# Kernel optimization log

Measured on AMD Instinct MI355X. Metric: run time of the kernel, lower is better.

The kernel has to match this reference:

```python
import jax, jax.numpy as jnp
import numpy as np

K = 3          # conv kernel size
STRIDE = 1     # conv stride (SAME padding)
ITERS = 3      # DR routing iterations
EPS = 1e-9     # squash epsilon


def squash(s, axis):
    # v = ||s||^2 / (1 + ||s||^2) * s / ||s||   (DR squash)
    sq = jnp.sum(s * s, axis=axis, keepdims=True)
    return (sq / (1.0 + sq)) * s * jax.lax.rsqrt(sq + EPS)


def setup_inputs() -> dict:
    key = jax.random.key(0)
    k1, k2, k3 = jax.random.split(key, 3)
    b, h, w, iCaps, iPose = 8, 12, 12, 32, 16
    oCaps, oPose = 32, 16
    x = jax.random.normal(k1, (b, h, w, iCaps, iPose), dtype=jnp.float32)
    # Wa: [kk*iCaps, oCaps, iPose, oPose] (leading 1 of the TF weight is dropped)
    fan = K * K * iCaps * iPose
    W = jax.random.normal(k2, (K * K * iCaps, oCaps, iPose, oPose), dtype=jnp.float32) * np.float32(np.sqrt(2.0 / fan))
    # biases: [oCaps, oPose] (TF shape [1,1,oCaps,oPose,1], broadcastable)
    biases = jax.random.normal(k3, (oCaps, oPose), dtype=jnp.float32) * 0.05
    return {"x": x, "W": W, "biases": biases}


def _kernel_tile(x2d):
    # im2col for SAME padding, stride 1.  x2d: (b, h, w, C) -> (b, h, w, k*k, C)
    b, h, w, C = x2d.shape
    pad = K // 2
    xp = jnp.pad(x2d, ((0, 0), (pad, pad), (pad, pad), (0, 0)))
    patches = jnp.stack(
        [xp[:, i:i + h, j:j + w, :] for i in range(K) for j in range(K)], axis=3
    )
    return patches  # (b, h, w, k*k, C)


def reference(x, W, biases):
    b, h, w, iCaps, iPose = x.shape
    iC = K * K * iCaps
    oC, oP = biases.shape

    # 1. kernel_tile: gather k*k neighborhoods
    patches = _kernel_tile(x.reshape(b, h, w, iCaps * iPose))      # (b,h,w,kk,iCaps*iPose)
    u = patches.reshape(b * h * w, iC, iPose)                       # (bx, iC, iPose)

    # 2. transform_view (vector capsules): votes[n,i,c,:] = u[n,i,:] @ W[i,c,:,:]
    votes = jnp.einsum('nip,icpq->nicq', u, W)                      # (bx, iC, oC, oP)

    # 3. DR routing
    bx = votes.shape[0]
    logits = jnp.zeros((bx, iC, oC), dtype=votes.dtype)
    v = None
    for ii in range(ITERS):
        c = jax.nn.softmax(logits, axis=2)                          # coupling coeffs over oCaps
        s = jnp.einsum('nic,nicq->ncq', c, votes) + biases          # (bx, oC, oP)
        v = squash(s, axis=2)
        if ii < ITERS - 1:
            logits = logits + jnp.einsum('nicq,ncq->nic', votes, v)  # agreement

    return v.reshape(b, h, w, oC, oP)
```

## Files before the change

kernel.cpp:

```cpp
#include <hip/hip_runtime.h>
#include <stdint.h>

typedef unsigned short ushort_t;

#define KK3 3
#define IC 32
#define IP 16
#define OC 32
#define OP 16
#define NI 288
#define HH 12
#define WWW 12
#define NTOT 1152
#define CQ 512
#define EPSQ 1e-9f
#define RWAVES 4
#define RSTEPS 36
#define NIP 144

typedef __attribute__((ext_vector_type(8))) short bf16x8;
typedef __attribute__((ext_vector_type(4))) float f32x4;

__device__ __forceinline__ float bf_lo(unsigned u) { return __uint_as_float(u << 16); }
__device__ __forceinline__ float bf_hi(unsigned u) { return __uint_as_float(u & 0xffff0000u); }
__device__ __forceinline__ ushort_t f2bf(float f) {
    unsigned u = __float_as_uint(f);
    return (ushort_t)((u + 0x7fffu + ((u >> 16) & 1u)) >> 16);
}

__global__ __launch_bounds__(64) void pack_kernel(
    const float* __restrict__ W, ushort_t* __restrict__ Wp)
{
    const int blk = blockIdx.x;
    const int ip = blk >> 5;
    const int c = blk & 31;
    const int l = threadIdx.x;
    const int i = ip * 2 + ((l >> 5) & 1);
    const int p0 = ((l >> 4) & 1) * 8;
    const int q = l & 15;
    const float* src = W + (((size_t)(i * 32 + c) * 16 + p0) * 16 + q);
    union { ushort_t s[8]; uint4 u4; } o;
#pragma unroll
    for (int j = 0; j < 8; ++j) o.s[j] = f2bf(src[(size_t)j * 16]);
    *(uint4*)(Wp + ((size_t)blk * 64 + l) * 8) = o.u4;
}

__global__ __launch_bounds__(256) void s0_gemm_kernel(
    const float* __restrict__ x, const ushort_t* __restrict__ Wp,
    float* __restrict__ s0_pre)
{
    __shared__ float red[4][512];

    const int t = threadIdx.x;
    const int wv = t >> 6;
    const int l = t & 63;
    const int pxt = blockIdx.x;
    const int ctb = blockIdx.y * 2;
    const int px = pxt * 16 + (l & 15);
    const int b = px / (HH * WWW);
    const int rem = px % (HH * WWW);
    const int y = rem / WWW;
    const int xx = rem % WWW;
    const int ioff = (l >> 5) & 1;
    const int p0 = ((l >> 4) & 1) * 8;

    f32x4 acc0 = (f32x4){0.f, 0.f, 0.f, 0.f};
    f32x4 acc1 = (f32x4){0.f, 0.f, 0.f, 0.f};

    const int ip0 = wv * (NIP / 4);
    for (int k = 0; k < NIP / 4; ++k) {
        const int ip = ip0 + k;
        const int i = ip * 2 + ioff;
        const int ky = i / (KK3 * IC);
        const int kx = (i / IC) % KK3;
        const int ic = i & (IC - 1);
        const int sy = y + ky - 1;
        const int sx = xx + kx - 1;
        union { ushort_t s[8]; bf16x8 v; } ua;
        if (sy >= 0 && sy < HH && sx >= 0 && sx < WWW) {
            const float* s = x + ((((size_t)b * HH + sy) * WWW + sx) * IC + ic) * IP + p0;
            const float4 v0 = *(const float4*)s;
            const float4 v1 = *(const float4*)(s + 4);
            ua.s[0] = f2bf(v0.x); ua.s[1] = f2bf(v0.y); ua.s[2] = f2bf(v0.z); ua.s[3] = f2bf(v0.w);
            ua.s[4] = f2bf(v1.x); ua.s[5] = f2bf(v1.y); ua.s[6] = f2bf(v1.z); ua.s[7] = f2bf(v1.w);
        } else {
#pragma unroll
            for (int j = 0; j < 8; ++j) ua.s[j] = 0;
        }
        const bf16x8 b0 = *(const bf16x8*)(Wp + (((size_t)ip * 32 + ctb) * 64 + l) * 8);
        const bf16x8 b1 = *(const bf16x8*)(Wp + (((size_t)ip * 32 + ctb + 1) * 64 + l) * 8);
        acc0 = __builtin_amdgcn_mfma_f32_16x16x32_bf16(ua.v, b0, acc0, 0, 0, 0);
        acc1 = __builtin_amdgcn_mfma_f32_16x16x32_bf16(ua.v, b1, acc1, 0, 0, 0);
    }

    {
        const int row = (l >> 4) * 4;
        const int col = l & 15;
#pragma unroll
        for (int r = 0; r < 4; ++r) {
            red[wv][(row + r) * 16 + col] = acc0[r];
            red[wv][256 + (row + r) * 16 + col] = acc1[r];
        }
    }
    __syncthreads();
#pragma unroll
    for (int rep = 0; rep < 2; ++rep) {
        const int k = t + rep * 256;
        const float v = (red[0][k] + red[1][k]) + (red[2][k] + red[3][k]);
        const int ct = k >> 8;
        const int row = (k >> 4) & 15;
        const int col = k & 15;
        s0_pre[(size_t)(pxt * 16 + row) * CQ + (size_t)(ctb + ct) * 16 + col] = v;
    }
}

__global__ __launch_bounds__(128) void votes_kernel(
    const float* __restrict__ x, const float* __restrict__ Wg,
    ushort_t* __restrict__ votes, int nStart, int nCount)
{
    __shared__ float u_lds[64][IP];

    const int i = blockIdx.x;
    const int tileBase = blockIdx.y * 64;
    const int nC = min(64, nCount - tileBase);
    const int t = threadIdx.x;
    const int c = t >> 2;
    const int qq = t & 3;

    const int ky = i / (KK3 * IC);
    const int kx = (i / IC) % KK3;
    const int ic = i % IC;

    {
        const int nl = t >> 1;
        const int ph = (t & 1) * 8;
        if (nl < nC) {
            const int n = nStart + tileBase + nl;
            const int b = n / (HH * WWW);
            const int rem = n % (HH * WWW);
            const int y = rem / WWW;
            const int xx = rem % WWW;
            const int sy = y + ky - 1;
            const int sx = xx + kx - 1;
            float4 v0 = make_float4(0.f, 0.f, 0.f, 0.f), v1 = v0;
            if (sy >= 0 && sy < HH && sx >= 0 && sx < WWW) {
                const float* src = x + ((((size_t)b * HH + sy) * WWW + sx) * IC + ic) * IP + ph;
                v0 = *(const float4*)(src);
                v1 = *(const float4*)(src + 4);
            }
            *(float4*)&u_lds[nl][ph] = v0;
            *(float4*)&u_lds[nl][ph + 4] = v1;
        }
    }

    float4 w[IP];
    {
        const float* wb = Wg + ((size_t)i * OC + c) * (IP * OP) + qq * 4;
#pragma unroll
        for (int p = 0; p < IP; ++p) w[p] = *(const float4*)(wb + p * OP);
    }
    __syncthreads();

    ushort_t* vb = votes + ((size_t)tileBase * NI + i) * CQ + c * OP + qq * 4;
    for (int nl = 0; nl < nC; ++nl) {
        const float4 u0 = *(const float4*)&u_lds[nl][0];
        const float4 u1 = *(const float4*)&u_lds[nl][4];
        const float4 u2 = *(const float4*)&u_lds[nl][8];
        const float4 u3 = *(const float4*)&u_lds[nl][12];
        float a0 = 0.f, a1 = 0.f, a2 = 0.f, a3 = 0.f;
#define ACC(uf, pp)                                         \
        a0 = fmaf(uf, w[pp].x, a0); a1 = fmaf(uf, w[pp].y, a1); \
        a2 = fmaf(uf, w[pp].z, a2); a3 = fmaf(uf, w[pp].w, a3);
        ACC(u0.x, 0)  ACC(u0.y, 1)  ACC(u0.z, 2)  ACC(u0.w, 3)
        ACC(u1.x, 4)  ACC(u1.y, 5)  ACC(u1.z, 6)  ACC(u1.w, 7)
        ACC(u2.x, 8)  ACC(u2.y, 9)  ACC(u2.z, 10) ACC(u2.w, 11)
        ACC(u3.x, 12) ACC(u3.y, 13) ACC(u3.z, 14) ACC(u3.w, 15)
#undef ACC
        ushort4 st;
        st.x = f2bf(a0); st.y = f2bf(a1); st.z = f2bf(a2); st.w = f2bf(a3);
        *(ushort4*)vb = st;
        vb += (size_t)NI * CQ;
    }
}

#define UNPACK16(A, B)                                                     \
    const float f0 = bf_lo(A.x), f1 = bf_hi(A.x), f2 = bf_lo(A.y),         \
                f3 = bf_hi(A.y), f4 = bf_lo(A.z), f5 = bf_hi(A.z),         \
                f6 = bf_lo(A.w), f7 = bf_hi(A.w), f8 = bf_lo(B.x),         \
                f9 = bf_hi(B.x), f10 = bf_lo(B.y), f11 = bf_hi(B.y),       \
                f12 = bf_lo(B.z), f13 = bf_hi(B.z), f14 = bf_lo(B.w),      \
                f15 = bf_hi(B.w);

__global__ __launch_bounds__(256) void route_kernel(
    const ushort_t* __restrict__ votes, const float* __restrict__ s0_pre,
    const float* __restrict__ bias, float* __restrict__ out, int nStart)
{
    __shared__ float lg_lds[NI * OC];
    __shared__ float sPart[RWAVES][CQ];
    __shared__ float s_sh[CQ];
    __shared__ float v_sh[CQ];
    __shared__ float fac_sh[OC];

    const int bn = blockIdx.x;
    const int t = threadIdx.x;
    const int wv = t >> 6;
    const int l = t & 63;
    const int isub = l >> 5;
    const int c = l & 31;
    const int iBase = 2 * wv + isub;

    const ushort_t* pbase = votes + (size_t)bn * NI * CQ + (size_t)iBase * CQ + c * OP;
    const size_t stepB = (size_t)8 * CQ;

#pragma unroll
    for (int rep = 0; rep < 2; ++rep) {
        const int k = t + rep * 256;
        s_sh[k] = fmaf(s0_pre[(size_t)(nStart + bn) * CQ + k], 1.0f / OC, bias[k]);
    }
    __syncthreads();
    if (t < OC) {
        float sq = 0.f;
#pragma unroll
        for (int q = 0; q < OP; ++q) { const float s = s_sh[t * OP + q]; sq = fmaf(s, s, sq); }
        fac_sh[t] = (sq / (1.0f + sq)) * rsqrtf(sq + EPSQ);
    }
    __syncthreads();
#pragma unroll
    for (int rep = 0; rep < 2; ++rep) {
        const int k = t + rep * 256;
        v_sh[k] = s_sh[k] * fac_sh[k >> 4];
    }
    __syncthreads();

    float sa[16];
    float vr[16];

#define RBODY(AA, BB, rr)                                                   \
        {                                                                   \
            UNPACK16(AA, BB)                                                \
            float a = f0 * vr[0];                                           \
            a = fmaf(f1, vr[1], a);   a = fmaf(f2, vr[2], a);               \
            a = fmaf(f3, vr[3], a);   a = fmaf(f4, vr[4], a);               \
            a = fmaf(f5, vr[5], a);   a = fmaf(f6, vr[6], a);               \
            a = fmaf(f7, vr[7], a);   a = fmaf(f8, vr[8], a);               \
            a = fmaf(f9, vr[9], a);   a = fmaf(f10, vr[10], a);             \
            a = fmaf(f11, vr[11], a); a = fmaf(f12, vr[12], a);             \
            a = fmaf(f13, vr[13], a); a = fmaf(f14, vr[14], a);             \
            a = fmaf(f15, vr[15], a);                                       \
            const int li = (iBase + 8 * (rr)) * OC + c;                     \
            if (it == 0) lg_lds[li] = a;                                    \
            else          a += lg_lds[li];                                  \
            const float e = __expf(a);                                      \
            float es = e;                                                   \
            es += __shfl_xor(es, 1);                                        \
            es += __shfl_xor(es, 2);                                        \
            es += __shfl_xor(es, 4);                                        \
            es += __shfl_xor(es, 8);                                        \
            es += __shfl_xor(es, 16);                                       \
            const float coup = __fdividef(e, es);                           \
            sa[0] = fmaf(coup, f0, sa[0]);   sa[1] = fmaf(coup, f1, sa[1]); \
            sa[2] = fmaf(coup, f2, sa[2]);   sa[3] = fmaf(coup, f3, sa[3]); \
            sa[4] = fmaf(coup, f4, sa[4]);   sa[5] = fmaf(coup, f5, sa[5]); \
            sa[6] = fmaf(coup, f6, sa[6]);   sa[7] = fmaf(coup, f7, sa[7]); \
            sa[8] = fmaf(coup, f8, sa[8]);   sa[9] = fmaf(coup, f9, sa[9]); \
            sa[10] = fmaf(coup, f10, sa[10]); sa[11] = fmaf(coup, f11, sa[11]); \
            sa[12] = fmaf(coup, f12, sa[12]); sa[13] = fmaf(coup, f13, sa[13]); \
            sa[14] = fmaf(coup, f14, sa[14]); sa[15] = fmaf(coup, f15, sa[15]); \
        }
#define RPREF(AA, BB, rn)                                                   \
        if ((rn) < RSTEPS) {                                                \
            const uint4* pn = (const uint4*)(pbase + (size_t)(rn) * stepB); \
            AA = pn[0]; BB = pn[1];                                         \
        }

#pragma unroll
    for (int it = 0; it < 2; ++it) {
#pragma unroll
        for (int k = 0; k < 4; ++k) {
            const float4 v4 = *(const float4*)&v_sh[c * 16 + 4 * k];
            vr[4*k] = v4.x; vr[4*k+1] = v4.y; vr[4*k+2] = v4.z; vr[4*k+3] = v4.w;
        }
#pragma unroll
        for (int q = 0; q < 16; ++q) sa[q] = 0.f;

        uint4 A0, B0, A1, B1, A2, B2;
        RPREF(A0, B0, 0)
        RPREF(A1, B1, 1)
        RPREF(A2, B2, 2)
        for (int r = 0; r < RSTEPS; r += 3) {
            RBODY(A0, B0, r)     RPREF(A0, B0, r + 3)
            RBODY(A1, B1, r + 1) RPREF(A1, B1, r + 4)
            RBODY(A2, B2, r + 2) RPREF(A2, B2, r + 5)
        }

#pragma unroll
        for (int q = 0; q < 16; ++q) sa[q] += __shfl_xor(sa[q], 32);
        if (isub == 0) {
#pragma unroll
            for (int k = 0; k < 4; ++k)
                *(float4*)&sPart[wv][c * 16 + 4 * k] = make_float4(sa[4*k], sa[4*k+1], sa[4*k+2], sa[4*k+3]);
        }
        __syncthreads();
#pragma unroll
        for (int rep = 0; rep < 2; ++rep) {
            const int k = t + rep * 256;
            float s = (sPart[0][k] + sPart[1][k]) + (sPart[2][k] + sPart[3][k]);
            s_sh[k] = s + bias[k];
        }
        __syncthreads();
        if (t < OC) {
            float sq = 0.f;
#pragma unroll
            for (int q = 0; q < OP; ++q) { const float s = s_sh[t * OP + q]; sq = fmaf(s, s, sq); }
            fac_sh[t] = (sq / (1.0f + sq)) * rsqrtf(sq + EPSQ);
        }
        __syncthreads();
#pragma unroll
        for (int rep = 0; rep < 2; ++rep) {
            const int k = t + rep * 256;
            v_sh[k] = s_sh[k] * fac_sh[k >> 4];
        }
        __syncthreads();
    }

#pragma unroll
    for (int rep = 0; rep < 2; ++rep) {
        const int k = t + rep * 256;
        out[(size_t)(nStart + bn) * CQ + k] = v_sh[k];
    }
}

extern "C" void kernel_launch(void* const* d_in, const int* in_sizes, int n_in,
                              void* d_out, int out_size, void* d_ws, size_t ws_size,
                              hipStream_t stream)
{
    const float* x = (const float*)d_in[0];
    const float* Wg = (const float*)d_in[1];
    const float* bias = (const float*)d_in[2];
    float* out = (float*)d_out;

    const size_t perN = (size_t)NI * CQ * sizeof(ushort_t);
    const size_t packBytes = (size_t)NIP * 32 * 64 * 8 * 2;
    const size_t s0Bytes = (size_t)NTOT * CQ * sizeof(float);

    int chunk = 576;
    if (ws_size < (size_t)chunk * perN + packBytes + s0Bytes) {
        size_t avail = (ws_size > packBytes + s0Bytes) ? ws_size - packBytes - s0Bytes : 0;
        chunk = (int)(avail / perN);
        if (chunk < 1) chunk = 1;
    }
    const size_t packOff = (size_t)chunk * perN;
    const size_t s0Off = packOff + packBytes;

    ushort_t* votes = (ushort_t*)d_ws;
    ushort_t* Wp = (ushort_t*)((char*)d_ws + packOff);
    float* s0_pre = (float*)((char*)d_ws + s0Off);

    hipLaunchKernelGGL(pack_kernel, dim3(NIP * 32), dim3(64), 0, stream, Wg, Wp);
    hipLaunchKernelGGL(s0_gemm_kernel, dim3(NTOT / 16, 16), dim3(256), 0, stream, x, Wp, s0_pre);

    for (int start = 0; start < NTOT; start += chunk) {
        const int cnt = (NTOT - start < chunk) ? (NTOT - start) : chunk;
        dim3 gA(NI, (cnt + 63) / 64);
        hipLaunchKernelGGL(votes_kernel, gA, dim3(128), 0, stream, x, Wg, votes, start, cnt);
        hipLaunchKernelGGL(route_kernel, dim3(cnt), dim3(256), 0, stream, votes, s0_pre, bias, out, start);
    }
}
```

Baseline: 260.8 us.

## Fuse vote computation into bf16 MFMA kernel that also produces s0 partials

Replaces the scalar-FMA votes kernel and the separate s0 GEMM with one MFMA kernel. Each block computes votes for 16 pixels over a group of input capsules, splitting the packed weight fragment into even/odd halves to get per-capsule votes, and writes them to bf16 through an LDS slab. It also accumulates the full s0 sum into partials that a new reduction kernel finishes. The chunk size also grows. In exchange it runs three MFMAs per fragment where one would do, adds two barriers per step, and needs extra workspace and a second pass for the s0 partials.

```diff
diff --git a/kernel.cpp b/kernel.cpp
--- a/kernel.cpp
+++ b/kernel.cpp
@@ -17,6 +17,8 @@
 #define RWAVES 4
 #define RSTEPS 36
 #define NIP 144
+#define NIG 18
+#define IPG 8
 
 typedef __attribute__((ext_vector_type(8))) short bf16x8;
 typedef __attribute__((ext_vector_type(4))) float f32x4;
@@ -45,141 +47,124 @@
     *(uint4*)(Wp + ((size_t)blk * 64 + l) * 8) = o.u4;
 }
 
-__global__ __launch_bounds__(256) void s0_gemm_kernel(
+__global__ __launch_bounds__(256) void votes_s0_kernel(
     const float* __restrict__ x, const ushort_t* __restrict__ Wp,
-    float* __restrict__ s0_pre)
-{
-    __shared__ float red[4][512];
+    ushort_t* __restrict__ votes, float* __restrict__ s0_part,
+    int nStart, int nCount)
+{
+    __shared__ float slab[2][16][CQ];
 
     const int t = threadIdx.x;
-    const int wv = t >> 6;
+    const int w = t >> 6;
     const int l = t & 63;
     const int pxt = blockIdx.x;
-    const int ctb = blockIdx.y * 2;
-    const int px = pxt * 16 + (l & 15);
-    const int b = px / (HH * WWW);
-    const int rem = px % (HH * WWW);
+    const int ig = blockIdx.y;
+
+    const int n = nStart + pxt * 16 + (l & 15);
+    const int b = n / (HH * WWW);
+    const int rem = n % (HH * WWW);
     const int y = rem / WWW;
     const int xx = rem % WWW;
     const int ioff = (l >> 5) & 1;
     const int p0 = ((l >> 4) & 1) * 8;
 
-    f32x4 acc0 = (f32x4){0.f, 0.f, 0.f, 0.f};
-    f32x4 acc1 = (f32x4){0.f, 0.f, 0.f, 0.f};
-
-    const int ip0 = wv * (NIP / 4);
-    for (int k = 0; k < NIP / 4; ++k) {
-        const int ip = ip0 + k;
-        const int i = ip * 2 + ioff;
-        const int ky = i / (KK3 * IC);
-        const int kx = (i / IC) % KK3;
-        const int ic = i & (IC - 1);
-        const int sy = y + ky - 1;
-        const int sx = xx + kx - 1;
+    const bf16x8 z8 = {0, 0, 0, 0, 0, 0, 0, 0};
+    const f32x4 z4 = {0.f, 0.f, 0.f, 0.f};
+
+    f32x4 accs0[8];
+#pragma unroll
+    for (int ctl = 0; ctl < 8; ++ctl) accs0[ctl] = z4;
+
+    for (int m = 0; m < IPG; ++m) {
+        const int ip = ig * IPG + m;
         union { ushort_t s[8]; bf16x8 v; } ua;
-        if (sy >= 0 && sy < HH && sx >= 0 && sx < WWW) {
-            const float* s = x + ((((size_t)b * HH + sy) * WWW + sx) * IC + ic) * IP + p0;
-            const float4 v0 = *(const float4*)s;
-            const float4 v1 = *(const float4*)(s + 4);
-            ua.s[0] = f2bf(v0.x); ua.s[1] = f2bf(v0.y); ua.s[2] = f2bf(v0.z); ua.s[3] = f2bf(v0.w);
-            ua.s[4] = f2bf(v1.x); ua.s[5] = f2bf(v1.y); ua.s[6] = f2bf(v1.z); ua.s[7] = f2bf(v1.w);
-        } else {
-#pragma unroll
-            for (int j = 0; j < 8; ++j) ua.s[j] = 0;
-        }
-        const bf16x8 b0 = *(const bf16x8*)(Wp + (((size_t)ip * 32 + ctb) * 64 + l) * 8);
-        const bf16x8 b1 = *(const bf16x8*)(Wp + (((size_t)ip * 32 + ctb + 1) * 64 + l) * 8);
-        acc0 = __builtin_amdgcn_mfma_f32_16x16x32_bf16(ua.v, b0, acc0, 0, 0, 0);
-        acc1 = __builtin_amdgcn_mfma_f32_16x16x32_bf16(ua.v, b1, acc1, 0, 0, 0);
+        {
+            const int i = ip * 2 + ioff;
+            const int ky = i / (KK3 * IC);
+            const int kx = (i / IC) % KK3;
+            const int ic = i & (IC - 1);
+            const int sy = y + ky - 1;
+            const int sx = xx + kx - 1;
+            if (sy >= 0 && sy < HH && sx >= 0 && sx < WWW) {
+                const float* s = x + ((((size_t)b * HH + sy) * WWW + sx) * IC + ic) * IP + p0;
+                const float4 v0 = *(const float4*)s;
+                const float4 v1 = *(const float4*)(s + 4);
+                ua.s[0] = f2bf(v0.x); ua.s[1] = f2bf(v0.y); ua.s[2] = f2bf(v0.z); ua.s[3] = f2bf(v0.w);
+                ua.s[4] = f2bf(v1.x); ua.s[5] = f2bf(v1.y); ua.s[6] = f2bf(v1.z); ua.s[7] = f2bf(v1.w);
+            } else {
+#pragma unroll
+                for (int j = 0; j < 8; ++j) ua.s[j] = 0;
+            }
+        }
+        const int q = l & 15;
+        const int r0 = (l >> 4) * 4;
+#pragma unroll
+        for (int ctl = 0; ctl < 8; ++ctl) {
+            const int ct = w * 8 + ctl;
+            const bf16x8 frag = *(const bf16x8*)(Wp + (((size_t)ip * 32 + ct) * 64 + l) * 8);
+            const bf16x8 be = (l < 32) ? frag : z8;
+            const bf16x8 bo = (l < 32) ? z8 : frag;
+            const f32x4 ve = __builtin_amdgcn_mfma_f32_16x16x32_bf16(ua.v, be, z4, 0, 0, 0);
+            const f32x4 vo = __builtin_amdgcn_mfma_f32_16x16x32_bf16(ua.v, bo, z4, 0, 0, 0);
+            accs0[ctl] = __builtin_amdgcn_mfma_f32_16x16x32_bf16(ua.v, frag, accs0[ctl], 0, 0, 0);
+            const int col = ct * 16 + q;
+#pragma unroll
+            for (int r = 0; r < 4; ++r) {
+                slab[0][r0 + r][col] = ve[r];
+                slab[1][r0 + r][col] = vo[r];
+            }
+        }
+        __syncthreads();
+        {
+            const int px = t >> 4;
+            const int ch0 = t & 15;
+            const int nl = pxt * 16 + px;
+#pragma unroll
+            for (int s = 0; s < 2; ++s) {
+                ushort_t* dst = votes + ((size_t)nl * NI + (2 * ip + s)) * CQ;
+#pragma unroll
+                for (int cc = 0; cc < 4; ++cc) {
+                    const int ch = ch0 + cc * 16;
+                    const float* sp = &slab[s][px][ch * 8];
+                    const float4 f0 = *(const float4*)sp;
+                    const float4 f1 = *(const float4*)(sp + 4);
+                    union { ushort_t s8[8]; uint4 u4; } o;
+                    o.s8[0] = f2bf(f0.x); o.s8[1] = f2bf(f0.y); o.s8[2] = f2bf(f0.z); o.s8[3] = f2bf(f0.w);
+                    o.s8[4] = f2bf(f1.x); o.s8[5] = f2bf(f1.y); o.s8[6] = f2bf(f1.z); o.s8[7] = f2bf(f1.w);
+                    *(uint4*)(dst + ch * 8) = o.u4;
+                }
+            }
+        }
+        __syncthreads();
     }
 
     {
-        const int row = (l >> 4) * 4;
-        const int col = l & 15;
-#pragma unroll
-        for (int r = 0; r < 4; ++r) {
-            red[wv][(row + r) * 16 + col] = acc0[r];
-            red[wv][256 + (row + r) * 16 + col] = acc1[r];
-        }
-    }
-    __syncthreads();
+        const int q = l & 15;
+        const int r0 = (l >> 4) * 4;
+#pragma unroll
+        for (int ctl = 0; ctl < 8; ++ctl) {
+            const int cq = (w * 8 + ctl) * 16 + q;
+#pragma unroll
+            for (int r = 0; r < 4; ++r)
+                s0_part[((size_t)ig * nCount + pxt * 16 + r0 + r) * CQ + cq] = accs0[ctl][r];
+        }
+    }
+}
+
+__global__ __launch_bounds__(256) void s0_fin_kernel(
+    const float* __restrict__ s0_part, float* __restrict__ s0_pre,
+    int nStart, int nCount)
+{
+    const int bn = blockIdx.x;
+    const int t = threadIdx.x;
 #pragma unroll
     for (int rep = 0; rep < 2; ++rep) {
         const int k = t + rep * 256;
-        const float v = (red[0][k] + red[1][k]) + (red[2][k] + red[3][k]);
-        const int ct = k >> 8;
-        const int row = (k >> 4) & 15;
-        const int col = k & 15;
-        s0_pre[(size_t)(pxt * 16 + row) * CQ + (size_t)(ctb + ct) * 16 + col] = v;
-    }
-}
-
-__global__ __launch_bounds__(128) void votes_kernel(
-    const float* __restrict__ x, const float* __restrict__ Wg,
-    ushort_t* __restrict__ votes, int nStart, int nCount)
-{
-    __shared__ float u_lds[64][IP];
-
-    const int i = blockIdx.x;
-    const int tileBase = blockIdx.y * 64;
-    const int nC = min(64, nCount - tileBase);
-    const int t = threadIdx.x;
-    const int c = t >> 2;
-    const int qq = t & 3;
-
-    const int ky = i / (KK3 * IC);
-    const int kx = (i / IC) % KK3;
-    const int ic = i % IC;
-
-    {
-        const int nl = t >> 1;
-        const int ph = (t & 1) * 8;
-        if (nl < nC) {
-            const int n = nStart + tileBase + nl;
-            const int b = n / (HH * WWW);
-            const int rem = n % (HH * WWW);
-            const int y = rem / WWW;
-            const int xx = rem % WWW;
-            const int sy = y + ky - 1;
-            const int sx = xx + kx - 1;
-            float4 v0 = make_float4(0.f, 0.f, 0.f, 0.f), v1 = v0;
-            if (sy >= 0 && sy < HH && sx >= 0 && sx < WWW) {
-                const float* src = x + ((((size_t)b * HH + sy) * WWW + sx) * IC + ic) * IP + ph;
-                v0 = *(const float4*)(src);
-                v1 = *(const float4*)(src + 4);
-            }
-            *(float4*)&u_lds[nl][ph] = v0;
-            *(float4*)&u_lds[nl][ph + 4] = v1;
-        }
-    }
-
-    float4 w[IP];
-    {
-        const float* wb = Wg + ((size_t)i * OC + c) * (IP * OP) + qq * 4;
-#pragma unroll
-        for (int p = 0; p < IP; ++p) w[p] = *(const float4*)(wb + p * OP);
-    }
-    __syncthreads();
-
-    ushort_t* vb = votes + ((size_t)tileBase * NI + i) * CQ + c * OP + qq * 4;
-    for (int nl = 0; nl < nC; ++nl) {
-        const float4 u0 = *(const float4*)&u_lds[nl][0];
-        const float4 u1 = *(const float4*)&u_lds[nl][4];
-        const float4 u2 = *(const float4*)&u_lds[nl][8];
-        const float4 u3 = *(const float4*)&u_lds[nl][12];
-        float a0 = 0.f, a1 = 0.f, a2 = 0.f, a3 = 0.f;
-#define ACC(uf, pp)                                         \
-        a0 = fmaf(uf, w[pp].x, a0); a1 = fmaf(uf, w[pp].y, a1); \
-        a2 = fmaf(uf, w[pp].z, a2); a3 = fmaf(uf, w[pp].w, a3);
-        ACC(u0.x, 0)  ACC(u0.y, 1)  ACC(u0.z, 2)  ACC(u0.w, 3)
-        ACC(u1.x, 4)  ACC(u1.y, 5)  ACC(u1.z, 6)  ACC(u1.w, 7)
-        ACC(u2.x, 8)  ACC(u2.y, 9)  ACC(u2.z, 10) ACC(u2.w, 11)
-        ACC(u3.x, 12) ACC(u3.y, 13) ACC(u3.z, 14) ACC(u3.w, 15)
-#undef ACC
-        ushort4 st;
-        st.x = f2bf(a0); st.y = f2bf(a1); st.z = f2bf(a2); st.w = f2bf(a3);
-        *(ushort4*)vb = st;
-        vb += (size_t)NI * CQ;
+        float s = 0.f;
+#pragma unroll
+        for (int g = 0; g < NIG; ++g)
+            s += s0_part[((size_t)g * nCount + bn) * CQ + k];
+        s0_pre[(size_t)(nStart + bn) * CQ + k] = s;
     }
 }
 
@@ -342,27 +327,33 @@
     const size_t perN = (size_t)NI * CQ * sizeof(ushort_t);
     const size_t packBytes = (size_t)NIP * 32 * 64 * 8 * 2;
     const size_t s0Bytes = (size_t)NTOT * CQ * sizeof(float);
-
-    int chunk = 576;
-    if (ws_size < (size_t)chunk * perN + packBytes + s0Bytes) {
+    const size_t perNpart = (size_t)NIG * CQ * sizeof(float);
+
+    int chunk = 768;
+    if (ws_size < (size_t)chunk * (perN + perNpart) + packBytes + s0Bytes) {
         size_t avail = (ws_size > packBytes + s0Bytes) ? ws_size - packBytes - s0Bytes : 0;
-        chunk = (int)(avail / perN);
-        if (chunk < 1) chunk = 1;
+        chunk = (int)(avail / (perN + perNpart));
+        chunk &= ~15;
+        if (chunk < 16) chunk = 16;
     }
     const size_t packOff = (size_t)chunk * perN;
     const size_t s0Off = packOff + packBytes;
+    const size_t partOff = s0Off + s0Bytes;
 
     ushort_t* votes = (ushort_t*)d_ws;
     ushort_t* Wp = (ushort_t*)((char*)d_ws + packOff);
     float* s0_pre = (float*)((char*)d_ws + s0Off);
+    float* s0_part = (float*)((char*)d_ws + partOff);
 
     hipLaunchKernelGGL(pack_kernel, dim3(NIP * 32), dim3(64), 0, stream, Wg, Wp);
-    hipLaunchKernelGGL(s0_gemm_kernel, dim3(NTOT / 16, 16), dim3(256), 0, stream, x, Wp, s0_pre);
 
     for (int start = 0; start < NTOT; start += chunk) {
         const int cnt = (NTOT - start < chunk) ? (NTOT - start) : chunk;
-        dim3 gA(NI, (cnt + 63) / 64);
-        hipLaunchKernelGGL(votes_kernel, gA, dim3(128), 0, stream, x, Wg, votes, start, cnt);
-        hipLaunchKernelGGL(route_kernel, dim3(cnt), dim3(256), 0, stream, votes, s0_pre, bias, out, start);
-    }
-}
+        hipLaunchKernelGGL(votes_s0_kernel, dim3(cnt / 16, NIG), dim3(256), 0, stream,
+                           x, Wp, votes, s0_part, start, cnt);
+        hipLaunchKernelGGL(s0_fin_kernel, dim3(cnt), dim3(256), 0, stream,
+                           s0_part, s0_pre, start, cnt);
+        hipLaunchKernelGGL(route_kernel, dim3(cnt), dim3(256), 0, stream,
+                           votes, s0_pre, bias, out, start);
+    }
+}
```

Result: faster. 215.0 us (-17.6%).
